# Kernel tuning notes

Measured on AMD Instinct MI355X. Metric: run time of the kernel, lower is better.

Reference implementation:

```python
import jax, jax.numpy as jnp
import numpy as np
from jax import lax

T = 50
THETA = 1.0 - 0.0001  # max_1 - 0.0001, max_1 = T_win/T = 1.0


def conv_t(x, w, b, pad_h):
    # x: [N, C, H, W, T]; slayer conv3d has time-kernel 1 -> conv2d per timestep.
    n, c, h, wd, t = x.shape
    xb = jnp.moveaxis(x, -1, 1).reshape(n * t, c, h, wd)
    y = lax.conv_general_dilated(xb, w, (1, 1), [(pad_h, pad_h), (0, 0)])
    y = y + b[None, :, None, None]
    o, h2, w2 = y.shape[1], y.shape[2], y.shape[3]
    return jnp.moveaxis(y.reshape(n, t, o, h2, w2), 1, -1)


def if_spikes(a):
    # catCuda.getSpikes on an input stacked T times: IF neuron with constant
    # drive a per step, soft reset (v -= theta on spike). a: [N,C,H,W].
    def step(v, _):
        v = v + a
        s = (v >= THETA).astype(a.dtype)
        return v - s * THETA, s
    _, sp = lax.scan(step, jnp.zeros_like(a), None, length=T)
    return jnp.moveaxis(sp, 0, -1)  # [N,C,H,W,T]


def setup_inputs() -> dict:
    key = jax.random.key(0)
    ks = jax.random.split(key, 6)
    def w(k, shape, scale):
        return jax.random.normal(k, shape, jnp.float32) * scale
    x = jax.random.uniform(ks[0], (256, 1, 180, 1, T), jnp.float32)
    return {
        'x': x,
        'w1': w(ks[1], (16, 1, 3, 1), 0.3), 'b1': jnp.zeros(16, jnp.float32),
        'w2': w(ks[2], (32, 16, 9, 1), 0.1), 'b2': jnp.zeros(32, jnp.float32),
        'w3': w(ks[3], (32, 32, 7, 1), 0.1), 'b3': jnp.zeros(32, jnp.float32),
        'wf': w(ks[4], (4, 32, 83, 1), 0.05), 'bf': jnp.zeros(4, jnp.float32),
    }


def reference(x, w1, b1, w2, b2, w3, b3, wf, bf):
    y = conv_t(x, w1, b1, 1)                        # [N,16,180,1,T]
    y = if_spikes(jnp.sum(y, axis=4) / T)           # rate -> spikes
    y = conv_t(y, w2, b2, 1)                        # [N,32,174,1,T]
    y = if_spikes(jnp.sum(y, axis=4) / T)
    y = 1.1 * (y[:, :, 0::2] + y[:, :, 1::2])       # slayer sum-pool (2,1), weight 1.1
    y = if_spikes(jnp.sum(y, axis=4) / T)           # [N,32,87,1,T]
    y = conv_t(y, w3, b3, 1)                        # [N,32,83,1,T]
    y = if_spikes(jnp.sum(y, axis=4) / T)
    out = jnp.einsum('nchwt,ochw->not', y, wf) + bf[None, :, None]  # dense over full spatial
    return jnp.sum(out, axis=-1) / T                # sum_spikes / T -> [N,4]
```

## Files before the change

kernel.cpp:

```cpp
#include <hip/hip_runtime.h>


#define T_STEPS 50
#define THETA   0.9999f

__device__ __forceinline__ float spike_rate(float a) {
    constexpr float INV = 50.0f / 0.9999f;
    float t = a * INV;
    float c = fminf(fmaxf(floorf(t), 0.0f), 50.0f);
    bool risky = (t > 0.5f) && (fabsf(t - rintf(t)) < 5e-4f);
    if (__ballot(risky)) {
        float v = 0.f, cnt = 0.f;
#pragma unroll 1
        for (int k = 0; k < T_STEPS; ++k) {
            v += a;
            float s = (v >= THETA) ? 1.0f : 0.0f;
            v -= s * THETA;
            cnt += s;
        }
        c = cnt;
    }
    return c / 50.0f;
}

extern "C" __global__ void __launch_bounds__(1024)
catnet_kernel(const float* __restrict__ x,
              const float* __restrict__ w1, const float* __restrict__ b1,
              const float* __restrict__ w2, const float* __restrict__ b2,
              const float* __restrict__ w3, const float* __restrict__ b3,
              const float* __restrict__ wf, const float* __restrict__ bf,
              float* __restrict__ out)
{
    const int n    = blockIdx.x;
    const int tid  = threadIdx.x;
    const int wave = tid >> 6;
    const int lane = tid & 63;

    __shared__ float xbar[182];
    __shared__ float r1p[16][182];
    __shared__ float r3p[32][89];
    __shared__ float r4s[32][83];
    __shared__ float part[16];

    if (tid < 16)              { r1p[tid][0] = 0.f; r1p[tid][181] = 0.f; }
    if (tid >= 32 && tid < 64) { r3p[tid-32][0] = 0.f; r3p[tid-32][88] = 0.f; }
    if (tid == 64)             { xbar[0] = 0.f; xbar[181] = 0.f; }

    const float* xn = x + (size_t)n * (180 * 50);
    if (tid < 720) {
        const int h = tid >> 2, q = tid & 3;
        const float* row = xn + h * 50;
        float s = 0.f;
        for (int t = q; t < T_STEPS; t += 4) s += row[t];
        s += __shfl_xor(s, 1, 4);
        s += __shfl_xor(s, 2, 4);
        if (q == 0) xbar[h + 1] = s;
    }
    __syncthreads();

    for (int idx = tid; idx < 16 * 180; idx += 1024) {
        int c = idx / 180, h = idx - c * 180;
        float a = w1[c*3+0] * xbar[h] + w1[c*3+1] * xbar[h+1] + w1[c*3+2] * xbar[h+2];
        a = a / 50.0f + b1[c];
        r1p[c][h + 1] = spike_rate(a);
    }
    __syncthreads();

    {
        const int g   = __builtin_amdgcn_readfirstlane(tid >> 7);
        const int p   = tid & 127;
        const bool act = p < 87;
        const int pr  = act ? p : 0;
        const float* wb = w2 + g * 4 * 144;

        float a0[4], a1[4];
#pragma unroll
        for (int j = 0; j < 4; ++j) { a0[j] = b2[g*4 + j]; a1[j] = a0[j]; }

        for (int ci = 0; ci < 16; ++ci) {
            float w[10];
#pragma unroll
            for (int d = 0; d < 10; ++d)
                w[d] = r1p[ci][2*pr + d];
#pragma unroll
            for (int j = 0; j < 4; ++j) {
                const float* wj = wb + j * 144 + ci * 9;
#pragma unroll
                for (int kh = 0; kh < 9; ++kh) {
                    float wv = wj[kh];
                    a0[j] += wv * w[kh];
                    a1[j] += wv * w[kh + 1];
                }
            }
        }
#pragma unroll
        for (int j = 0; j < 4; ++j) {
            float r20 = spike_rate(a0[j]);
            float r21 = spike_rate(a1[j]);
            float r3  = spike_rate(1.1f * (r20 + r21));
            if (act) r3p[g*4 + j][p + 1] = r3;
        }
    }
    __syncthreads();

    {
        const int g4   = __builtin_amdgcn_readfirstlane((wave >> 1) * 4);
        const int half = wave & 1;
        const int cnt  = half ? 41 : 42;
        const bool act = lane < cnt;
        const int h0   = half * 42 + lane;
        const int hr   = act ? h0 : 0;
        const float* wb = w3 + g4 * 224;

        float a[4];
#pragma unroll
        for (int j = 0; j < 4; ++j) a[j] = b3[g4 + j];

        for (int ci = 0; ci < 32; ++ci) {
            float rv[7];
#pragma unroll
            for (int kh = 0; kh < 7; ++kh) rv[kh] = r3p[ci][hr + kh];
#pragma unroll
            for (int j = 0; j < 4; ++j) {
                const float* wj = wb + j * 224 + ci * 7;
#pragma unroll
                for (int kh = 0; kh < 7; ++kh)
                    a[j] += wj[kh] * rv[kh];
            }
        }
#pragma unroll
        for (int j = 0; j < 4; ++j) {
            float r = spike_rate(a[j]);
            if (act) r4s[g4 + j][h0] = r;
        }
    }
    __syncthreads();

    {
        const int o = wave >> 2, q = wave & 3;
        const float* r4f = &r4s[0][0];
        const float* wo  = wf + o * (32 * 83);
        float acc = 0.f;
        for (int j = q * 64 + lane; j < 32 * 83; j += 256)
            acc += r4f[j] * wo[j];
#pragma unroll
        for (int off = 32; off > 0; off >>= 1)
            acc += __shfl_down(acc, off, 64);
        if (lane == 0) part[wave] = acc;
    }
    __syncthreads();
    if (tid < 4) {
        float s = part[tid*4] + part[tid*4+1] + part[tid*4+2] + part[tid*4+3];
        out[n * 4 + tid] = s + bf[tid];
    }
}

extern "C" void kernel_launch(void* const* d_in, const int* in_sizes, int n_in,
                              void* d_out, int out_size, void* d_ws, size_t ws_size,
                              hipStream_t stream) {
    const float* x  = (const float*)d_in[0];
    const float* w1 = (const float*)d_in[1];
    const float* b1 = (const float*)d_in[2];
    const float* w2 = (const float*)d_in[3];
    const float* b2 = (const float*)d_in[4];
    const float* w3 = (const float*)d_in[5];
    const float* b3 = (const float*)d_in[6];
    const float* wf = (const float*)d_in[7];
    const float* bf = (const float*)d_in[8];
    float* outp = (float*)d_out;

    catnet_kernel<<<dim3(256), dim3(1024), 0, stream>>>(
        x, w1, b1, w2, b2, w3, b3, wf, bf, outp);
}
```

Measured before the change: 104.3 us.

## Split layer-1 rates into even/odd arrays and widen conv3 channel groups

After: 108.2 us. 3.7% more time.

```diff
diff --git a/kernel.cpp b/kernel.cpp
--- a/kernel.cpp
+++ b/kernel.cpp
@@ -37,12 +37,13 @@
     const int lane = tid & 63;
 
     __shared__ float xbar[182];
-    __shared__ float r1p[16][182];
+    __shared__ float r1e[16][91];
+    __shared__ float r1o[16][91];
     __shared__ float r3p[32][89];
     __shared__ float r4s[32][83];
     __shared__ float part[16];
 
-    if (tid < 16)              { r1p[tid][0] = 0.f; r1p[tid][181] = 0.f; }
+    if (tid < 16)              { r1e[tid][0] = 0.f; r1o[tid][90] = 0.f; }
     if (tid >= 32 && tid < 64) { r3p[tid-32][0] = 0.f; r3p[tid-32][88] = 0.f; }
     if (tid == 64)             { xbar[0] = 0.f; xbar[181] = 0.f; }
 
@@ -62,7 +63,10 @@
         int c = idx / 180, h = idx - c * 180;
         float a = w1[c*3+0] * xbar[h] + w1[c*3+1] * xbar[h+1] + w1[c*3+2] * xbar[h+2];
         a = a / 50.0f + b1[c];
-        r1p[c][h + 1] = spike_rate(a);
+        float r = spike_rate(a);
+        int pidx = h + 1;
+        float* dst = (pidx & 1) ? &r1o[c][pidx >> 1] : &r1e[c][pidx >> 1];
+        *dst = r;
     }
     __syncthreads();
 
@@ -78,19 +82,21 @@
         for (int j = 0; j < 4; ++j) { a0[j] = b2[g*4 + j]; a1[j] = a0[j]; }
 
         for (int ci = 0; ci < 16; ++ci) {
-            float w[10];
+            float we[5], wo[5];
 #pragma unroll
-            for (int d = 0; d < 10; ++d)
-                w[d] = r1p[ci][2*pr + d];
+            for (int d = 0; d < 5; ++d) {
+                we[d] = r1e[ci][pr + d];
+                wo[d] = r1o[ci][pr + d];
+            }
 #pragma unroll
             for (int j = 0; j < 4; ++j) {
                 const float* wj = wb + j * 144 + ci * 9;
-#pragma unroll
-                for (int kh = 0; kh < 9; ++kh) {
-                    float wv = wj[kh];
-                    a0[j] += wv * w[kh];
-                    a1[j] += wv * w[kh + 1];
-                }
+                a0[j] += wj[0]*we[0] + wj[1]*wo[0] + wj[2]*we[1] + wj[3]*wo[1]
+                       + wj[4]*we[2] + wj[5]*wo[2] + wj[6]*we[3] + wj[7]*wo[3]
+                       + wj[8]*we[4];
+                a1[j] += wj[0]*wo[0] + wj[1]*we[1] + wj[2]*wo[1] + wj[3]*we[2]
+                       + wj[4]*wo[2] + wj[5]*we[3] + wj[6]*wo[3] + wj[7]*we[4]
+                       + wj[8]*wo[4];
             }
         }
 #pragma unroll
@@ -103,35 +109,34 @@
     }
     __syncthreads();
 
-    {
-        const int g4   = __builtin_amdgcn_readfirstlane((wave >> 1) * 4);
+    if (wave < 8) {
+        const int g8   = __builtin_amdgcn_readfirstlane((wave >> 1) * 8);
         const int half = wave & 1;
         const int cnt  = half ? 41 : 42;
         const bool act = lane < cnt;
         const int h0   = half * 42 + lane;
         const int hr   = act ? h0 : 0;
-        const float* wb = w3 + g4 * 224;
 
-        float a[4];
+        float a[8];
 #pragma unroll
-        for (int j = 0; j < 4; ++j) a[j] = b3[g4 + j];
+        for (int j = 0; j < 8; ++j) a[j] = b3[g8 + j];
 
         for (int ci = 0; ci < 32; ++ci) {
             float rv[7];
 #pragma unroll
             for (int kh = 0; kh < 7; ++kh) rv[kh] = r3p[ci][hr + kh];
 #pragma unroll
-            for (int j = 0; j < 4; ++j) {
-                const float* wj = wb + j * 224 + ci * 7;
+            for (int j = 0; j < 8; ++j) {
+                const float* wj = w3 + ((g8 + j) * 32 + ci) * 7;
 #pragma unroll
                 for (int kh = 0; kh < 7; ++kh)
                     a[j] += wj[kh] * rv[kh];
             }
         }
 #pragma unroll
-        for (int j = 0; j < 4; ++j) {
+        for (int j = 0; j < 8; ++j) {
             float r = spike_rate(a[j]);
-            if (act) r4s[g4 + j][h0] = r;
+            if (act) r4s[g8 + j][h0] = r;
         }
     }
     __syncthreads();
```
